# Optimization experiments

Measured on AMD Instinct MI355X. Metric: run time of the kernel, lower is better.

The kernel has to match this reference:

```python
import jax, jax.numpy as jnp
import numpy as np

N_GROUPS = 32
N_HEADS = 8
GN_EPS = 1e-5


def setup_inputs() -> dict:
    key = jax.random.key(0)
    k1, k2, k3 = jax.random.split(key, 3)
    B, C, H, W = 8, 512, 32, 32
    x = jax.random.normal(k1, (B, C, H, W), dtype=jnp.float32)
    gn_w = jnp.ones((C,), dtype=jnp.float32)
    gn_b = jnp.zeros((C,), dtype=jnp.float32)
    qkv_w = jax.random.normal(k2, (3 * C, C), dtype=jnp.float32) * 0.02
    qkv_b = jnp.zeros((3 * C,), dtype=jnp.float32)
    proj_w = jax.random.normal(k3, (C, C), dtype=jnp.float32) * 0.02
    proj_b = jnp.zeros((C,), dtype=jnp.float32)
    return {"x": x, "gn_w": gn_w, "gn_b": gn_b, "qkv_w": qkv_w,
            "qkv_b": qkv_b, "proj_w": proj_w, "proj_b": proj_b}


def reference(x, gn_w, gn_b, qkv_w, qkv_b, proj_w, proj_b):
    b, c, h, w = x.shape
    t = h * w
    xf = x.reshape(b, c, t)

    # GroupNorm(32, C) over (channel-group, spatial) dims
    xg = xf.reshape(b, N_GROUPS, (c // N_GROUPS) * t)
    mean = jnp.mean(xg, axis=-1, keepdims=True)
    var = jnp.var(xg, axis=-1, keepdims=True)
    normed = ((xg - mean) * jax.lax.rsqrt(var + GN_EPS)).reshape(b, c, t)
    normed = normed * gn_w[None, :, None] + gn_b[None, :, None]

    # 1x1 Conv1d -> matmul over channel dim
    qkv = jnp.einsum('oc,bct->bot', qkv_w, normed) + qkv_b[None, :, None]
    q, k, v = jnp.split(qkv, 3, axis=1)  # each [b, c, t]

    ch = c // N_HEADS
    scale = 1.0 / np.sqrt(np.sqrt(ch)).astype(np.float32)
    q = (q * scale).reshape(b * N_HEADS, ch, t)
    k = (k * scale).reshape(b * N_HEADS, ch, t)
    v = v.reshape(b * N_HEADS, ch, t)

    weight = jnp.einsum('bct,bcs->bts', q, k)
    weight = jax.nn.softmax(weight.astype(jnp.float32), axis=-1).astype(q.dtype)
    a = jnp.einsum('bts,bcs->bct', weight, v).reshape(b, c, t)

    # residual + 1x1 Conv2d projection
    out = jnp.einsum('oc,bct->bot', proj_w, xf + a) + proj_b[None, :, None]
    return out.reshape(b, -1, h, w)
```

## Files before the change

kernel.cpp:

```cpp
#include <hip/hip_runtime.h>

constexpr int B = 8;
constexpr int C = 512;
constexpr int T = 1024;
constexpr int CPG = 16;
constexpr int NH = 8;
constexpr int CH = 64;
constexpr float GN_EPS = 1e-5f;
constexpr float QSCALE = 0.18033688011112042f;

typedef __attribute__((ext_vector_type(4))) float f32x4;
typedef __attribute__((ext_vector_type(8))) short bf16x8;
typedef __attribute__((ext_vector_type(4))) short bf16x4;

__device__ inline short f2bf(float f) {
  union { float f; unsigned u; } v; v.f = f;
  unsigned r = (v.u + 0x7FFFu + ((v.u >> 16) & 1u)) >> 16;
  return (short)r;
}

__device__ inline unsigned cvt_pk_bf16(float a, float b) {
  unsigned r;
  asm("v_cvt_pk_bf16_f32 %0, %1, %2" : "=v"(r) : "v"(a), "v"(b));
  return r;
}

#define GLOAD16(gsrc, ldst) __builtin_amdgcn_global_load_lds( \
    (const __attribute__((address_space(1))) unsigned int*)(gsrc), \
    (__attribute__((address_space(3))) unsigned int*)(ldst), 16, 0, 0)

__global__ __launch_bounds__(256)
void wconv_kernel(const float* __restrict__ qw, const float* __restrict__ pw,
                  short* __restrict__ qwb, short* __restrict__ pwb) {
  const int idx = blockIdx.x * 256 + threadIdx.x;
  constexpr int QW4 = 3 * C * C / 4;
  float4 v;
  short* dst;
  if (idx < QW4) {
    v = ((const float4*)qw)[idx];
    dst = qwb + (size_t)idx * 4;
  } else {
    v = ((const float4*)pw)[idx - QW4];
    dst = pwb + (size_t)(idx - QW4) * 4;
  }
  bf16x4 o;
  o[0] = f2bf(v.x); o[1] = f2bf(v.y); o[2] = f2bf(v.z); o[3] = f2bf(v.w);
  *(bf16x4*)dst = o;
}

__global__ __launch_bounds__(256)
void gn_kernel(const float* __restrict__ x, const float* __restrict__ gw,
               const float* __restrict__ gb, short* __restrict__ out) {
  const int b = blockIdx.x >> 5;
  const int g = blockIdx.x & 31;
  const float* xp = x + (size_t)(b * C + g * CPG) * T;
  const float4* x4 = (const float4*)xp;
  float s = 0.f, ss = 0.f;
  for (int i = threadIdx.x; i < CPG * T / 4; i += 256) {
    float4 v = x4[i];
    s  += v.x + v.y + v.z + v.w;
    ss += v.x * v.x + v.y * v.y + v.z * v.z + v.w * v.w;
  }
  #pragma unroll
  for (int o = 32; o; o >>= 1) {
    s  += __shfl_down(s, o);
    ss += __shfl_down(ss, o);
  }
  __shared__ float rs[4], rss[4];
  __shared__ float sm, sr;
  const int wid = threadIdx.x >> 6;
  if ((threadIdx.x & 63) == 0) { rs[wid] = s; rss[wid] = ss; }
  __syncthreads();
  if (threadIdx.x == 0) {
    float ts  = rs[0] + rs[1] + rs[2] + rs[3];
    float tss = rss[0] + rss[1] + rss[2] + rss[3];
    constexpr float inv_n = 1.f / (CPG * T);
    float mean = ts * inv_n;
    float var = tss * inv_n - mean * mean;
    sm = mean;
    sr = rsqrtf(var + GN_EPS);
  }
  __syncthreads();
  const float mean = sm, rstd = sr;

  const int tid = threadIdx.x;
  const int cl = tid >> 4;
  const int t4 = (tid & 15) * 4;
  const float cw = gw[g * CPG + cl] * rstd;
  const float cb = gb[g * CPG + cl] - mean * cw;
  __shared__ short tile[64][20];
  const int tr = tid >> 2;
  const int cq = (tid & 3) * 4;
  for (int t0 = 0; t0 < T; t0 += 64) {
    float4 v = x4[(cl * T + t0 + t4) >> 2];
    tile[t4 + 0][cl] = f2bf(v.x * cw + cb);
    tile[t4 + 1][cl] = f2bf(v.y * cw + cb);
    tile[t4 + 2][cl] = f2bf(v.z * cw + cb);
    tile[t4 + 3][cl] = f2bf(v.w * cw + cb);
    __syncthreads();
    *(bf16x4*)&out[((size_t)(b * T + t0 + tr)) * C + g * CPG + cq] =
        *(const bf16x4*)&tile[tr][cq];
    __syncthreads();
  }
}

__global__ __launch_bounds__(256)
void qkv_gemm(const short* __restrict__ Wb, const float* __restrict__ bias,
              const short* __restrict__ Xn, short* __restrict__ qb,
              short* __restrict__ kb, short* __restrict__ vb) {
  const int b = blockIdx.z;
  const int o0 = blockIdx.y * 128;
  const int t0 = blockIdx.x * 128;
  const bool swap = (o0 >= 2 * C);
  __shared__ short Asm[2][128 * 64];
  __shared__ short Bsm[2][128 * 64];
  const int tid = threadIdx.x;
  const int wv = tid >> 6, lane = tid & 63;
  const int l15 = lane & 15, l4 = lane >> 4;
  const int wr = (wv >> 1) * 64, wc = (wv & 1) * 64;

  const short* gA[4]; const short* gB[4];
  char* lA[4]; char* lB[4];
  #pragma unroll
  for (int p = 0; p < 4; ++p) {
    const int off = p * 256 + tid;
    const int row = off >> 3;
    const int col = (off & 7) ^ (row & 7);
    gA[p] = Wb + (size_t)(o0 + row) * C + col * 8;
    gB[p] = Xn + ((size_t)b * T + t0 + row) * C + col * 8;
    lA[p] = (char*)&Asm[0][0] + (size_t)(p * 256 + (tid & ~63)) * 16;
    lB[p] = (char*)&Bsm[0][0] + (size_t)(p * 256 + (tid & ~63)) * 16;
  }

  f32x4 acc[4][4];
  #pragma unroll
  for (int i = 0; i < 4; ++i)
    #pragma unroll
    for (int j = 0; j < 4; ++j) acc[i][j] = f32x4{0.f, 0.f, 0.f, 0.f};

  #pragma unroll
  for (int p = 0; p < 4; ++p) {
    GLOAD16(gA[p], lA[p]);
    GLOAD16(gB[p], lB[p]);
  }
  __syncthreads();

  int cur = 0;
  for (int ks = 0; ks < 8; ++ks) {
    if (ks < 7) {
      const int k0n = (ks + 1) * 64;
      #pragma unroll
      for (int p = 0; p < 4; ++p) {
        GLOAD16(gA[p] + k0n, lA[p] + (cur ^ 1) * 16384);
        GLOAD16(gB[p] + k0n, lB[p] + (cur ^ 1) * 16384);
      }
    }
    const short* As = &Asm[cur][0];
    const short* Bs = &Bsm[cur][0];
    #pragma unroll
    for (int kk = 0; kk < 2; ++kk) {
      bf16x8 af[4], bfr[4];
      #pragma unroll
      for (int i = 0; i < 4; ++i) {
        const int sw = ((kk << 2) | l4) ^ (l15 & 7);
        af[i]  = *(const bf16x8*)&As[(wr + i * 16 + l15) * 64 + sw * 8];
        bfr[i] = *(const bf16x8*)&Bs[(wc + i * 16 + l15) * 64 + sw * 8];
      }
      __builtin_amdgcn_s_setprio(1);
      if (!swap) {
        #pragma unroll
        for (int fi = 0; fi < 4; ++fi)
          #pragma unroll
          for (int nj = 0; nj < 4; ++nj)
            acc[fi][nj] = __builtin_amdgcn_mfma_f32_16x16x32_bf16(
                af[fi], bfr[nj], acc[fi][nj], 0, 0, 0);
      } else {
        #pragma unroll
        for (int nj = 0; nj < 4; ++nj)
          #pragma unroll
          for (int fi = 0; fi < 4; ++fi)
            acc[nj][fi] = __builtin_amdgcn_mfma_f32_16x16x32_bf16(
                bfr[nj], af[fi], acc[nj][fi], 0, 0, 0);
      }
      __builtin_amdgcn_s_setprio(0);
    }
    __syncthreads();
    cur ^= 1;
  }

  if (!swap) {
    short* dst = (o0 < C) ? qb : kb;
    const float sc = (o0 < C) ? QSCALE : 1.0f;
    #pragma unroll
    for (int fi = 0; fi < 4; ++fi) {
      const int ob = o0 + wr + fi * 16 + l4 * 4;
      const int bh = b * NH + ((ob >> 6) & 7);
      const int cb_ = ob & 63;
      #pragma unroll
      for (int nj = 0; nj < 4; ++nj) {
        const int tg = t0 + wc + nj * 16 + l15;
        bf16x4 pk;
        #pragma unroll
        for (int r = 0; r < 4; ++r)
          pk[r] = f2bf((acc[fi][nj][r] + bias[ob + r]) * sc);
        *(bf16x4*)&dst[((size_t)bh * T + tg) * CH + cb_] = pk;
      }
    }
  } else {
    #pragma unroll
    for (int fi = 0; fi < 4; ++fi) {
      const int ob = o0 + wr + fi * 16 + l15;
      const int bh = b * NH + ((ob >> 6) & 7);
      const int cb_ = ob & 63;
      const float bo = bias[ob];
      #pragma unroll
      for (int nj = 0; nj < 4; ++nj) {
        const int tg = t0 + wc + nj * 16 + l4 * 4;
        bf16x4 pk;
        #pragma unroll
        for (int r = 0; r < 4; ++r)
          pk[r] = f2bf(acc[nj][fi][r] + bo);
        *(bf16x4*)&vb[((size_t)bh * CH + cb_) * T + tg] = pk;
      }
    }
  }
}

__global__ __launch_bounds__(256)
void attn_kernel(const short* __restrict__ qb, const short* __restrict__ kb,
                 const short* __restrict__ vb, const float* __restrict__ x,
                 short* __restrict__ res) {
  const int bh = blockIdx.x & 63;
  const int tile = blockIdx.x >> 6;
  const int b = bh >> 3, h = bh & 7;
  const int t0 = tile * 128;
  const int tid = threadIdx.x;
  const int wv = tid >> 6;
  const int lane = tid & 63;
  const int l15 = lane & 15;
  const int l4 = lane >> 4;

  const short* qh = qb + (size_t)bh * T * CH;
  const short* kh = kb + (size_t)bh * T * CH;
  const short* vh = vb + (size_t)bh * CH * T;

  __shared__ short kt[2][64][64];
  __shared__ short vt[2][64][64];
  __shared__ short pl[4][2][16][64];
  short* plw = &pl[wv][0][0][0];

  const int sl_row[2] = { (0 * 256 + tid) >> 3, (1 * 256 + tid) >> 3 };
  const int sl_blk[2] = { (tid & 7) ^ (sl_row[0] & 7), (tid & 7) ^ (sl_row[1] & 7) };
  const int sl_lds[2] = { (0 * 256 + (tid & ~63)) * 8, (1 * 256 + (tid & ~63)) * 8 };

  bf16x8 qf[2][2];
  #pragma unroll
  for (int nj = 0; nj < 2; ++nj)
    #pragma unroll
    for (int ks = 0; ks < 2; ++ks)
      qf[nj][ks] = *(const bf16x8*)
          &qh[(size_t)(t0 + wv * 32 + nj * 16 + l15) * CH + ks * 32 + l4 * 8];

  f32x4 acc_o[2][4];
  #pragma unroll
  for (int nj = 0; nj < 2; ++nj)
    #pragma unroll
    for (int ct = 0; ct < 4; ++ct) acc_o[nj][ct] = f32x4{0.f, 0.f, 0.f, 0.f};
  float lsum[2] = {0.f, 0.f};

  #pragma unroll
  for (int p = 0; p < 2; ++p) {
    GLOAD16(kh + (size_t)sl_row[p] * CH + sl_blk[p] * 8, (char*)&kt[0][0][0] + sl_lds[p] * 2);
    GLOAD16(vh + (size_t)sl_row[p] * T + sl_blk[p] * 8, (char*)&vt[0][0][0] + sl_lds[p] * 2);
  }

  for (int it = 0; it < 16; ++it) {
    const int cur = it & 1;
    __syncthreads();
    if (it < 15) {
      const int s1 = (it + 1) * 64;
      #pragma unroll
      for (int p = 0; p < 2; ++p) {
        GLOAD16(kh + (size_t)(s1 + sl_row[p]) * CH + sl_blk[p] * 8,
                (char*)&kt[cur ^ 1][0][0] + sl_lds[p] * 2);
        GLOAD16(vh + (size_t)sl_row[p] * T + s1 + sl_blk[p] * 8,
                (char*)&vt[cur ^ 1][0][0] + sl_lds[p] * 2);
      }
    }
    const short* ktc = &kt[cur][0][0];
    const short* vtc = &vt[cur][0][0];

    f32x4 accs[2][4];
    #pragma unroll
    for (int nj = 0; nj < 2; ++nj)
      #pragma unroll
      for (int nt = 0; nt < 4; ++nt) accs[nj][nt] = f32x4{0.f, 0.f, 0.f, 0.f};
    __builtin_amdgcn_s_setprio(1);
    #pragma unroll
    for (int ks = 0; ks < 2; ++ks) {
      #pragma unroll
      for (int nt = 0; nt < 4; ++nt) {
        bf16x8 kf = *(const bf16x8*)
            &ktc[(nt * 16 + l15) * 64 + (((ks << 2) | l4) ^ (l15 & 7)) * 8];
        accs[0][nt] = __builtin_amdgcn_mfma_f32_16x16x32_bf16(kf, qf[0][ks], accs[0][nt], 0, 0, 0);
        accs[1][nt] = __builtin_amdgcn_mfma_f32_16x16x32_bf16(kf, qf[1][ks], accs[1][nt], 0, 0, 0);
      }
    }
    __builtin_amdgcn_s_setprio(0);

    f32x4 p4[2][4];
    #pragma unroll
    for (int nj = 0; nj < 2; ++nj) {
      #pragma unroll
      for (int nt = 0; nt < 4; ++nt)
        #pragma unroll
        for (int r = 0; r < 4; ++r)
          p4[nj][nt][r] = __builtin_amdgcn_exp2f(accs[nj][nt][r]);
      f32x4 sv;
      #pragma unroll
      for (int r = 0; r < 4; ++r)
        sv[r] = (p4[nj][0][r] + p4[nj][1][r]) + (p4[nj][2][r] + p4[nj][3][r]);
      lsum[nj] += (sv[0] + sv[1]) + (sv[2] + sv[3]);
      #pragma unroll
      for (int nt = 0; nt < 4; ++nt) {
        uint2 w;
        w.x = cvt_pk_bf16(p4[nj][nt][0], p4[nj][nt][1]);
        w.y = cvt_pk_bf16(p4[nj][nt][2], p4[nj][nt][3]);
        *(uint2*)&plw[nj * 1024 + l15 * 64 +
                      ((nt * 2 + (l4 >> 1)) ^ (l15 & 7)) * 8 + (l4 & 1) * 4] = w;
      }
    }

    __builtin_amdgcn_s_setprio(1);
    #pragma unroll
    for (int ks = 0; ks < 2; ++ks) {
      const int psl = (((ks << 2) | l4) ^ (l15 & 7)) * 8;
      bf16x8 pf0 = *(const bf16x8*)&plw[l15 * 64 + psl];
      bf16x8 pf1 = *(const bf16x8*)&plw[1024 + l15 * 64 + psl];
      #pragma unroll
      for (int ct = 0; ct < 4; ++ct) {
        bf16x8 vf = *(const bf16x8*)
            &vtc[(ct * 16 + l15) * 64 + (((ks << 2) | l4) ^ (l15 & 7)) * 8];
        acc_o[0][ct] = __builtin_amdgcn_mfma_f32_16x16x32_bf16(vf, pf0, acc_o[0][ct], 0, 0, 0);
        acc_o[1][ct] = __builtin_amdgcn_mfma_f32_16x16x32_bf16(vf, pf1, acc_o[1][ct], 0, 0, 0);
      }
    }
    __builtin_amdgcn_s_setprio(0);
  }

  #pragma unroll
  for (int nj = 0; nj < 2; ++nj) {
    float l = lsum[nj];
    l += __shfl_xor(l, 16);
    l += __shfl_xor(l, 32);
    const float inv = 1.f / l;
    const int trow = t0 + wv * 32 + nj * 16 + l15;
    #pragma unroll
    for (int ct = 0; ct < 4; ++ct) {
      const int cbase = h * CH + ct * 16 + l4 * 4;
      bf16x4 pk;
      #pragma unroll
      for (int r = 0; r < 4; ++r) {
        const float xv = x[((size_t)(b * C + cbase + r)) * T + trow];
        pk[r] = f2bf(acc_o[nj][ct][r] * inv + xv);
      }
      *(bf16x4*)&res[((size_t)(b * T + trow)) * C + cbase] = pk;
    }
  }
}

__global__ __launch_bounds__(256)
void proj_gemm(const short* __restrict__ Wp, const float* __restrict__ bias,
               const short* __restrict__ Rs, float* __restrict__ out) {
  const int b = blockIdx.z;
  const int o0 = blockIdx.y * 128;
  const int t0 = blockIdx.x * 128;
  __shared__ short Asm[2][128 * 64];
  __shared__ short Bsm[2][128 * 64];
  const int tid = threadIdx.x;
  const int wv = tid >> 6, lane = tid & 63;
  const int l15 = lane & 15, l4 = lane >> 4;
  const int wr = (wv >> 1) * 64, wc = (wv & 1) * 64;

  const short* gA[4]; const short* gB[4];
  char* lA[4]; char* lB[4];
  #pragma unroll
  for (int p = 0; p < 4; ++p) {
    const int off = p * 256 + tid;
    const int row = off >> 3;
    const int col = (off & 7) ^ (row & 7);
    gA[p] = Wp + (size_t)(o0 + row) * C + col * 8;
    gB[p] = Rs + ((size_t)b * T + t0 + row) * C + col * 8;
    lA[p] = (char*)&Asm[0][0] + (size_t)(p * 256 + (tid & ~63)) * 16;
    lB[p] = (char*)&Bsm[0][0] + (size_t)(p * 256 + (tid & ~63)) * 16;
  }

  f32x4 acc[4][4];
  #pragma unroll
  for (int i = 0; i < 4; ++i)
    #pragma unroll
    for (int j = 0; j < 4; ++j) acc[i][j] = f32x4{0.f, 0.f, 0.f, 0.f};

  #pragma unroll
  for (int p = 0; p < 4; ++p) {
    GLOAD16(gA[p], lA[p]);
    GLOAD16(gB[p], lB[p]);
  }
  __syncthreads();

  int cur = 0;
  for (int ks = 0; ks < 8; ++ks) {
    if (ks < 7) {
      const int k0n = (ks + 1) * 64;
      #pragma unroll
      for (int p = 0; p < 4; ++p) {
        GLOAD16(gA[p] + k0n, lA[p] + (cur ^ 1) * 16384);
        GLOAD16(gB[p] + k0n, lB[p] + (cur ^ 1) * 16384);
      }
    }
    const short* As = &Asm[cur][0];
    const short* Bs = &Bsm[cur][0];
    #pragma unroll
    for (int kk = 0; kk < 2; ++kk) {
      bf16x8 af[4], bfr[4];
      #pragma unroll
      for (int i = 0; i < 4; ++i) {
        const int sw = ((kk << 2) | l4) ^ (l15 & 7);
        af[i]  = *(const bf16x8*)&As[(wr + i * 16 + l15) * 64 + sw * 8];
        bfr[i] = *(const bf16x8*)&Bs[(wc + i * 16 + l15) * 64 + sw * 8];
      }
      __builtin_amdgcn_s_setprio(1);
      #pragma unroll
      for (int nj = 0; nj < 4; ++nj)
        #pragma unroll
        for (int fi = 0; fi < 4; ++fi)
          acc[nj][fi] = __builtin_amdgcn_mfma_f32_16x16x32_bf16(
              bfr[nj], af[fi], acc[nj][fi], 0, 0, 0);
      __builtin_amdgcn_s_setprio(0);
    }
    __syncthreads();
    cur ^= 1;
  }

  #pragma unroll
  for (int fi = 0; fi < 4; ++fi) {
    const int o = o0 + wr + fi * 16 + l15;
    const float bo = bias[o];
    #pragma unroll
    for (int nj = 0; nj < 4; ++nj) {
      const int tg = t0 + wc + nj * 16 + l4 * 4;
      f32x4 vo;
      #pragma unroll
      for (int r = 0; r < 4; ++r) vo[r] = acc[nj][fi][r] + bo;
      *(f32x4*)&out[((size_t)(b * C + o)) * T + tg] = vo;
    }
  }
}

extern "C" void kernel_launch(void* const* d_in, const int* in_sizes, int n_in,
                              void* d_out, int out_size, void* d_ws, size_t ws_size,
                              hipStream_t stream) {
  const float* x      = (const float*)d_in[0];
  const float* gn_w   = (const float*)d_in[1];
  const float* gn_b   = (const float*)d_in[2];
  const float* qkv_w  = (const float*)d_in[3];
  const float* qkv_b  = (const float*)d_in[4];
  const float* proj_w = (const float*)d_in[5];
  const float* proj_b = (const float*)d_in[6];
  float* out = (float*)d_out;

  constexpr size_t MB = 1 << 20;
  char* w = (char*)d_ws;
  short* normed = (short*)w;
  short* qbuf   = (short*)(w + 8 * MB);
  short* kbuf   = (short*)(w + 16 * MB);
  short* vbuf   = (short*)(w + 24 * MB);
  short* resb   = (short*)(w + 32 * MB);
  short* qwb    = (short*)(w + 40 * MB);
  short* pwb    = (short*)(w + 40 * MB + (size_t)3 * C * C * 2);

  wconv_kernel<<<dim3(1024), 256, 0, stream>>>(qkv_w, proj_w, qwb, pwb);
  gn_kernel<<<dim3(B * 32), 256, 0, stream>>>(x, gn_w, gn_b, normed);
  qkv_gemm<<<dim3(T / 128, 3 * C / 128, B), 256, 0, stream>>>(qwb, qkv_b, normed,
                                                              qbuf, kbuf, vbuf);
  attn_kernel<<<dim3(B * NH * (T / 128)), 256, 0, stream>>>(qbuf, kbuf, vbuf, x, resb);
  proj_gemm<<<dim3(T / 128, C / 128, B), 256, 0, stream>>>(pwb, proj_b, resb, out);
}
```

Measured before the change: 93.59 us.

## Single-buffer GEMM LDS and remap block indices to 1D batch-interleaved grid

Result: faster. 90.92 us (-2.8%).

```diff
diff --git a/kernel.cpp b/kernel.cpp
--- a/kernel.cpp
+++ b/kernel.cpp
@@ -108,12 +108,14 @@
 void qkv_gemm(const short* __restrict__ Wb, const float* __restrict__ bias,
               const short* __restrict__ Xn, short* __restrict__ qb,
               short* __restrict__ kb, short* __restrict__ vb) {
-  const int b = blockIdx.z;
-  const int o0 = blockIdx.y * 128;
-  const int t0 = blockIdx.x * 128;
+  const int bid = blockIdx.x;
+  const int b = bid & 7;
+  const int rem = bid >> 3;
+  const int o0 = (rem % 12) * 128;
+  const int t0 = (rem / 12) * 128;
   const bool swap = (o0 >= 2 * C);
-  __shared__ short Asm[2][128 * 64];
-  __shared__ short Bsm[2][128 * 64];
+  __shared__ short Asm[128 * 64];
+  __shared__ short Bsm[128 * 64];
   const int tid = threadIdx.x;
   const int wv = tid >> 6, lane = tid & 63;
   const int l15 = lane & 15, l4 = lane >> 4;
@@ -128,8 +130,8 @@
     const int col = (off & 7) ^ (row & 7);
     gA[p] = Wb + (size_t)(o0 + row) * C + col * 8;
     gB[p] = Xn + ((size_t)b * T + t0 + row) * C + col * 8;
-    lA[p] = (char*)&Asm[0][0] + (size_t)(p * 256 + (tid & ~63)) * 16;
-    lB[p] = (char*)&Bsm[0][0] + (size_t)(p * 256 + (tid & ~63)) * 16;
+    lA[p] = (char*)Asm + (size_t)(p * 256 + (tid & ~63)) * 16;
+    lB[p] = (char*)Bsm + (size_t)(p * 256 + (tid & ~63)) * 16;
   }
 
   f32x4 acc[4][4];
@@ -138,35 +140,22 @@
     #pragma unroll
     for (int j = 0; j < 4; ++j) acc[i][j] = f32x4{0.f, 0.f, 0.f, 0.f};
 
-  #pragma unroll
-  for (int p = 0; p < 4; ++p) {
-    GLOAD16(gA[p], lA[p]);
-    GLOAD16(gB[p], lB[p]);
-  }
-  __syncthreads();
-
-  int cur = 0;
-  for (int ks = 0; ks < 8; ++ks) {
-    if (ks < 7) {
-      const int k0n = (ks + 1) * 64;
-      #pragma unroll
-      for (int p = 0; p < 4; ++p) {
-        GLOAD16(gA[p] + k0n, lA[p] + (cur ^ 1) * 16384);
-        GLOAD16(gB[p] + k0n, lB[p] + (cur ^ 1) * 16384);
-      }
-    }
-    const short* As = &Asm[cur][0];
-    const short* Bs = &Bsm[cur][0];
+  for (int k0 = 0; k0 < C; k0 += 64) {
+    #pragma unroll
+    for (int p = 0; p < 4; ++p) {
+      GLOAD16(gA[p] + k0, lA[p]);
+      GLOAD16(gB[p] + k0, lB[p]);
+    }
+    __syncthreads();
     #pragma unroll
     for (int kk = 0; kk < 2; ++kk) {
       bf16x8 af[4], bfr[4];
       #pragma unroll
       for (int i = 0; i < 4; ++i) {
         const int sw = ((kk << 2) | l4) ^ (l15 & 7);
-        af[i]  = *(const bf16x8*)&As[(wr + i * 16 + l15) * 64 + sw * 8];
-        bfr[i] = *(const bf16x8*)&Bs[(wc + i * 16 + l15) * 64 + sw * 8];
-      }
-      __builtin_amdgcn_s_setprio(1);
+        af[i]  = *(const bf16x8*)&Asm[(wr + i * 16 + l15) * 64 + sw * 8];
+        bfr[i] = *(const bf16x8*)&Bsm[(wc + i * 16 + l15) * 64 + sw * 8];
+      }
       if (!swap) {
         #pragma unroll
         for (int fi = 0; fi < 4; ++fi)
@@ -182,10 +171,8 @@
             acc[nj][fi] = __builtin_amdgcn_mfma_f32_16x16x32_bf16(
                 bfr[nj], af[fi], acc[nj][fi], 0, 0, 0);
       }
-      __builtin_amdgcn_s_setprio(0);
-    }
-    __syncthreads();
-    cur ^= 1;
+    }
+    __syncthreads();
   }
 
   if (!swap) {
@@ -372,11 +359,13 @@
 __global__ __launch_bounds__(256)
 void proj_gemm(const short* __restrict__ Wp, const float* __restrict__ bias,
                const short* __restrict__ Rs, float* __restrict__ out) {
-  const int b = blockIdx.z;
-  const int o0 = blockIdx.y * 128;
-  const int t0 = blockIdx.x * 128;
-  __shared__ short Asm[2][128 * 64];
-  __shared__ short Bsm[2][128 * 64];
+  const int bid = blockIdx.x;
+  const int b = bid & 7;
+  const int rem = bid >> 3;
+  const int o0 = (rem % 4) * 128;
+  const int t0 = (rem / 4) * 128;
+  __shared__ short Asm[128 * 64];
+  __shared__ short Bsm[128 * 64];
   const int tid = threadIdx.x;
   const int wv = tid >> 6, lane = tid & 63;
   const int l15 = lane & 15, l4 = lane >> 4;
@@ -391,8 +380,8 @@
     const int col = (off & 7) ^ (row & 7);
     gA[p] = Wp + (size_t)(o0 + row) * C + col * 8;
     gB[p] = Rs + ((size_t)b * T + t0 + row) * C + col * 8;
-    lA[p] = (char*)&Asm[0][0] + (size_t)(p * 256 + (tid & ~63)) * 16;
-    lB[p] = (char*)&Bsm[0][0] + (size_t)(p * 256 + (tid & ~63)) * 16;
+    lA[p] = (char*)Asm + (size_t)(p * 256 + (tid & ~63)) * 16;
+    lB[p] = (char*)Bsm + (size_t)(p * 256 + (tid & ~63)) * 16;
   }
 
   f32x4 acc[4][4];
@@ -401,45 +390,30 @@
     #pragma unroll
     for (int j = 0; j < 4; ++j) acc[i][j] = f32x4{0.f, 0.f, 0.f, 0.f};
 
-  #pragma unroll
-  for (int p = 0; p < 4; ++p) {
-    GLOAD16(gA[p], lA[p]);
-    GLOAD16(gB[p], lB[p]);
-  }
-  __syncthreads();
-
-  int cur = 0;
-  for (int ks = 0; ks < 8; ++ks) {
-    if (ks < 7) {
-      const int k0n = (ks + 1) * 64;
-      #pragma unroll
-      for (int p = 0; p < 4; ++p) {
-        GLOAD16(gA[p] + k0n, lA[p] + (cur ^ 1) * 16384);
-        GLOAD16(gB[p] + k0n, lB[p] + (cur ^ 1) * 16384);
-      }
-    }
-    const short* As = &Asm[cur][0];
-    const short* Bs = &Bsm[cur][0];
+  for (int k0 = 0; k0 < C; k0 += 64) {
+    #pragma unroll
+    for (int p = 0; p < 4; ++p) {
+      GLOAD16(gA[p] + k0, lA[p]);
+      GLOAD16(gB[p] + k0, lB[p]);
+    }
+    __syncthreads();
     #pragma unroll
     for (int kk = 0; kk < 2; ++kk) {
       bf16x8 af[4], bfr[4];
       #pragma unroll
       for (int i = 0; i < 4; ++i) {
         const int sw = ((kk << 2) | l4) ^ (l15 & 7);
-        af[i]  = *(const bf16x8*)&As[(wr + i * 16 + l15) * 64 + sw * 8];
-        bfr[i] = *(const bf16x8*)&Bs[(wc + i * 16 + l15) * 64 + sw * 8];
-      }
-      __builtin_amdgcn_s_setprio(1);
+        af[i]  = *(const bf16x8*)&Asm[(wr + i * 16 + l15) * 64 + sw * 8];
+        bfr[i] = *(const bf16x8*)&Bsm[(wc + i * 16 + l15) * 64 + sw * 8];
+      }
       #pragma unroll
       for (int nj = 0; nj < 4; ++nj)
         #pragma unroll
         for (int fi = 0; fi < 4; ++fi)
           acc[nj][fi] = __builtin_amdgcn_mfma_f32_16x16x32_bf16(
               bfr[nj], af[fi], acc[nj][fi], 0, 0, 0);
-      __builtin_amdgcn_s_setprio(0);
-    }
-    __syncthreads();
-    cur ^= 1;
+    }
+    __syncthreads();
   }
 
   #pragma unroll
@@ -481,8 +455,7 @@
 
   wconv_kernel<<<dim3(1024), 256, 0, stream>>>(qkv_w, proj_w, qwb, pwb);
   gn_kernel<<<dim3(B * 32), 256, 0, stream>>>(x, gn_w, gn_b, normed);
-  qkv_gemm<<<dim3(T / 128, 3 * C / 128, B), 256, 0, stream>>>(qwb, qkv_b, normed,
-                                                              qbuf, kbuf, vbuf);
+  qkv_gemm<<<dim3(768), 256, 0, stream>>>(qwb, qkv_b, normed, qbuf, kbuf, vbuf);
   attn_kernel<<<dim3(B * NH * (T / 128)), 256, 0, stream>>>(qbuf, kbuf, vbuf, x, resb);
-  proj_gemm<<<dim3(T / 128, C / 128, B), 256, 0, stream>>>(pwb, proj_b, resb, out);
-}
+  proj_gemm<<<dim3(256), 256, 0, stream>>>(pwb, proj_b, resb, out);
+}
```
